# Performance work log

Measured on AMD Instinct MI355X. Metric: run time of the kernel, lower is better.

Reference implementation:

```python
import jax, jax.numpy as jnp
import numpy as np

EMB = 64
HID = 128
N_NODES = 50000
N_EDGES = 800000
N_Q = 64

def setup_inputs() -> dict:
    key = jax.random.key(0)
    ks = jax.random.split(key, 20)
    d = {}
    d['question_emb'] = jax.random.normal(ks[0], (N_Q, EMB), dtype=jnp.float32)
    d['node_embeddings'] = jax.random.normal(ks[1], (N_NODES, EMB), dtype=jnp.float32)
    d['edge_embeddings'] = jax.random.normal(ks[2], (N_EDGES, EMB), dtype=jnp.float32)
    d['edge_index'] = jax.random.randint(ks[3], (2, N_EDGES), 0, N_NODES, dtype=jnp.int32)
    d['node_batch'] = jnp.sort(jax.random.randint(ks[4], (N_NODES,), 0, N_Q, dtype=jnp.int32))
    s = 1.0 / np.sqrt(EMB)
    # projector weights (Linear emb->emb), stored as (in, out)
    d['Wq'] = jax.random.normal(ks[5], (EMB, EMB), dtype=jnp.float32) * s
    d['bq'] = jnp.zeros((EMB,), dtype=jnp.float32)
    d['We'] = jax.random.normal(ks[6], (EMB, EMB), dtype=jnp.float32) * s
    d['be'] = jnp.zeros((EMB,), dtype=jnp.float32)
    d['Wr'] = jax.random.normal(ks[7], (EMB, EMB), dtype=jnp.float32) * s
    d['br'] = jnp.zeros((EMB,), dtype=jnp.float32)
    # DenseFeatureExtractor: concat(4*EMB) -> EMB -> HID, ReLU after each
    d['W1'] = jax.random.normal(ks[8], (4 * EMB, EMB), dtype=jnp.float32) / np.sqrt(4 * EMB)
    d['b1'] = jnp.zeros((EMB,), dtype=jnp.float32)
    d['W2'] = jax.random.normal(ks[9], (EMB, HID), dtype=jnp.float32) * s
    d['b2'] = jnp.zeros((HID,), dtype=jnp.float32)
    # DeterministicHead: HID -> 1
    d['Wh'] = jax.random.normal(ks[10], (HID, 1), dtype=jnp.float32) / np.sqrt(HID)
    d['bh'] = jnp.zeros((1,), dtype=jnp.float32)
    return d


def reference(question_emb, node_embeddings, edge_embeddings, edge_index, node_batch,
              Wq, bq, We, be, Wr, br, W1, b1, W2, b2, Wh, bh):
    head_idx, tail_idx = edge_index[0], edge_index[1]
    query_ids = node_batch[head_idx]                       # [E]
    # projections (applied to the small tables, then gathered per edge)
    q_repr = question_emb @ Wq + bq                        # [Q, D]
    node_repr = node_embeddings @ We + be                  # [N, D]
    rel_repr = edge_embeddings @ Wr + br                   # [E, D]
    semantic = jnp.concatenate([
        q_repr[query_ids], node_repr[head_idx], rel_repr, node_repr[tail_idx]
    ], axis=-1)                                            # [E, 4D]
    h = jax.nn.relu(semantic @ W1 + b1)                    # [E, D]
    h = jax.nn.relu(h @ W2 + b2)                           # [E, H]
    logits = (h @ Wh + bh)[:, 0]                           # [E]
    scores = jax.nn.sigmoid(logits)
    return scores
```

## Files before the change

### kernel.cpp

```cpp
#include <hip/hip_runtime.h>

#define NNODE 50000
#define NEDGE 800000

typedef __attribute__((ext_vector_type(8))) short bf16x8;
typedef __attribute__((ext_vector_type(4))) float f32x4;

#define WB_QCB   0
#define WB_WRTB  8192
#define WB_W2TB  16384
#define WB_WEH   33024
#define WB_WET   49408
#define WB_NHB   65792
#define WB_NTB   6465792

__device__ inline ushort f2b(float x) {
    uint u = __float_as_uint(x);
    return (ushort)((u + 0x7fffu + ((u >> 16) & 1u)) >> 16);
}
__device__ inline uint cvtpk(float lo, float hi) {
    uint r;
    asm("v_cvt_pk_bf16_f32 %0, %1, %2" : "=v"(r) : "v"(lo), "v"(hi));
    return r;
}
__device__ inline float bLo(uint u) { return __uint_as_float(u << 16); }
__device__ inline float bHi(uint u) { return __uint_as_float(u & 0xffff0000u); }

__device__ inline void stage64(float* dst, const float* __restrict__ src, int t) {
    #pragma unroll
    for (int i = 0; i < 4; ++i) {
        int f = t + i * 256;
        *(float4*)&dst[f * 4] = *(const float4*)&src[f * 4];
    }
}

__device__ inline void gemm64(const float* sA, const float* sB, int t, float acc[4][4]) {
    const int r0 = (t >> 4) * 4, c0 = (t & 15) * 4;
    #pragma unroll
    for (int j = 0; j < 4; ++j)
        #pragma unroll
        for (int i = 0; i < 4; ++i) acc[j][i] = 0.f;
    #pragma unroll 4
    for (int k = 0; k < 64; ++k) {
        float4 b = *(const float4*)&sB[k * 64 + c0];
        float bv[4] = {b.x, b.y, b.z, b.w};
        #pragma unroll
        for (int j = 0; j < 4; ++j) {
            float a = sA[(r0 + j) * 64 + k];
            #pragma unroll
            for (int i = 0; i < 4; ++i) acc[j][i] = fmaf(a, bv[i], acc[j][i]);
        }
    }
}

__global__ __launch_bounds__(256)
void prep_small(const float* __restrict__ Q,
                const float* __restrict__ Wq, const float* __restrict__ bq,
                const float* __restrict__ We, const float* __restrict__ be,
                const float* __restrict__ Wr, const float* __restrict__ br,
                const float* __restrict__ W1, const float* __restrict__ b1,
                const float* __restrict__ W2, char* __restrict__ wsb)
{
    __shared__ float sA[4096], sB[4096], sC[4096], sBias[64];
    const int t = threadIdx.x;
    const int bid = blockIdx.x;
    const int r0 = (t >> 4) * 4, c0 = (t & 15) * 4;

    if (bid == 0) {
        stage64(sA, Wq, t); stage64(sB, W1, t);
        __syncthreads();
        float acc[4][4];
        gemm64(sA, sB, t, acc);
        #pragma unroll
        for (int j = 0; j < 4; ++j)
            *(float4*)&sC[(r0 + j) * 64 + c0] = make_float4(acc[j][0], acc[j][1], acc[j][2], acc[j][3]);
        if (t < 64) {
            float s = b1[t];
            for (int k = 0; k < 64; ++k) {
                s = fmaf(bq[k], W1[k * 64 + t], s);
                s = fmaf(be[k], W1[(64 + k) * 64 + t] + W1[(192 + k) * 64 + t], s);
                s = fmaf(br[k], W1[(128 + k) * 64 + t], s);
            }
            sBias[t] = s;
        }
        __syncthreads();
        stage64(sA, Q, t);
        __syncthreads();
        gemm64(sA, sC, t, acc);
        ushort* qcb = (ushort*)(wsb + WB_QCB);
        #pragma unroll
        for (int j = 0; j < 4; ++j) {
            ushort4 p;
            p.x = f2b(acc[j][0] + sBias[c0 + 0]);
            p.y = f2b(acc[j][1] + sBias[c0 + 1]);
            p.z = f2b(acc[j][2] + sBias[c0 + 2]);
            p.w = f2b(acc[j][3] + sBias[c0 + 3]);
            *(ushort4*)&qcb[(r0 + j) * 64 + c0] = p;
        }
    } else if (bid == 1 || bid == 2) {
        const float* w1seg = W1 + (bid == 1 ? 64 * 64 : 192 * 64);
        float* dst = (float*)(wsb + (bid == 1 ? WB_WEH : WB_WET));
        stage64(sA, We, t); stage64(sB, w1seg, t);
        __syncthreads();
        float acc[4][4];
        gemm64(sA, sB, t, acc);
        #pragma unroll
        for (int j = 0; j < 4; ++j)
            *(float4*)&dst[(r0 + j) * 64 + c0] = make_float4(acc[j][0], acc[j][1], acc[j][2], acc[j][3]);
    } else if (bid == 3) {
        stage64(sA, Wr, t); stage64(sB, W1 + 128 * 64, t);
        __syncthreads();
        float acc[4][4];
        gemm64(sA, sB, t, acc);
        ushort* wrtb = (ushort*)(wsb + WB_WRTB);
        #pragma unroll
        for (int j = 0; j < 4; ++j)
            #pragma unroll
            for (int i = 0; i < 4; ++i)
                wrtb[(c0 + i) * 64 + (r0 + j)] = f2b(acc[j][i]);
    } else {
        ushort* w2tb = (ushort*)(wsb + WB_W2TB);
        #pragma unroll
        for (int i = 0; i < 32; ++i) {
            int f = t + i * 256;
            int k = f >> 7, n = f & 127;
            w2tb[n * 64 + k] = f2b(W2[f]);
        }
    }
}

__global__ __launch_bounds__(256)
void prep_nodes(const float* __restrict__ Xn, const char* __restrict__ wsb_c,
                char* __restrict__ wsb)
{
    __shared__ float sXT[64 * 68];
    __shared__ float sWeh[4096], sWet[4096];
    const int t = threadIdx.x;
    const int nbase = blockIdx.x * 64;
    const float* Weh = (const float*)(wsb_c + WB_WEH);
    const float* Wet = (const float*)(wsb_c + WB_WET);
    ushort* nhb = (ushort*)(wsb + WB_NHB);
    ushort* ntb = (ushort*)(wsb + WB_NTB);

    #pragma unroll
    for (int i = 0; i < 4; ++i) {
        int f = t + i * 256;
        int n = f >> 4, s4 = (f & 15) * 4;
        int gn = nbase + n;
        float4 v = make_float4(0.f, 0.f, 0.f, 0.f);
        if (gn < NNODE) v = *(const float4*)&Xn[gn * 64 + s4];
        sXT[(s4 + 0) * 68 + n] = v.x;
        sXT[(s4 + 1) * 68 + n] = v.y;
        sXT[(s4 + 2) * 68 + n] = v.z;
        sXT[(s4 + 3) * 68 + n] = v.w;
    }
    #pragma unroll
    for (int i = 0; i < 4; ++i) {
        int f = t + i * 256;
        *(float4*)&sWeh[f * 4] = *(const float4*)&Weh[f * 4];
        *(float4*)&sWet[f * 4] = *(const float4*)&Wet[f * 4];
    }
    __syncthreads();

    const int er = (t >> 4) * 4, cc = (t & 15) * 4;
    float ah[4][4], at[4][4];
    #pragma unroll
    for (int j = 0; j < 4; ++j)
        #pragma unroll
        for (int i = 0; i < 4; ++i) { ah[j][i] = 0.f; at[j][i] = 0.f; }
    #pragma unroll 4
    for (int k = 0; k < 64; ++k) {
        float4 a  = *(const float4*)&sXT[k * 68 + er];
        float4 bh = *(const float4*)&sWeh[k * 64 + cc];
        float4 bt = *(const float4*)&sWet[k * 64 + cc];
        float av[4] = {a.x, a.y, a.z, a.w};
        #pragma unroll
        for (int j = 0; j < 4; ++j) {
            ah[j][0] = fmaf(av[j], bh.x, ah[j][0]); ah[j][1] = fmaf(av[j], bh.y, ah[j][1]);
            ah[j][2] = fmaf(av[j], bh.z, ah[j][2]); ah[j][3] = fmaf(av[j], bh.w, ah[j][3]);
            at[j][0] = fmaf(av[j], bt.x, at[j][0]); at[j][1] = fmaf(av[j], bt.y, at[j][1]);
            at[j][2] = fmaf(av[j], bt.z, at[j][2]); at[j][3] = fmaf(av[j], bt.w, at[j][3]);
        }
    }
    #pragma unroll
    for (int j = 0; j < 4; ++j) {
        int n = nbase + er + j;
        if (n < NNODE) {
            uint2 ph, pt;
            ph.x = cvtpk(ah[j][0], ah[j][1]); ph.y = cvtpk(ah[j][2], ah[j][3]);
            pt.x = cvtpk(at[j][0], at[j][1]); pt.y = cvtpk(at[j][2], at[j][3]);
            *(uint2*)&nhb[n * 64 + cc] = ph;
            *(uint2*)&ntb[n * 64 + cc] = pt;
        }
    }
}

#define TILES_PER_BLK 4

__global__ __launch_bounds__(256, 2)
void edge_kernel(const float* __restrict__ Xe,
                 const int* __restrict__ EI,
                 const int* __restrict__ NB,
                 const float* __restrict__ b2,
                 const float* __restrict__ Wh,
                 const float* __restrict__ bh,
                 const char* __restrict__ wsb,
                 float* __restrict__ out)
{
    __shared__ ushort sX[64 * 72];
    __shared__ ushort sG[64 * 72];

    const int t = threadIdx.x;
    const ushort* qcb  = (const ushort*)(wsb + WB_QCB);
    const ushort* wrtb = (const ushort*)(wsb + WB_WRTB);
    const ushort* w2tb = (const ushort*)(wsb + WB_W2TB);
    const ushort* nhb  = (const ushort*)(wsb + WB_NHB);
    const ushort* ntb  = (const ushort*)(wsb + WB_NTB);

    const int lane = t & 63;
    const int w    = t >> 6;
    const int m    = lane & 15;
    const int qq   = lane >> 4;
    const int q8   = qq * 8;

    const int eg  = t >> 2;
    const int c0g = (t & 3) * 16;
    const int xrow = 16 * w + (lane >> 2);
    const int xsl  = lane & 3;

    bf16x8 wrF[4][2], w2F[8][2];
    #pragma unroll
    for (int nt = 0; nt < 4; ++nt) {
        wrF[nt][0] = *(const bf16x8*)&wrtb[(nt * 16 + m) * 64 + q8];
        wrF[nt][1] = *(const bf16x8*)&wrtb[(nt * 16 + m) * 64 + 32 + q8];
    }
    #pragma unroll
    for (int nt = 0; nt < 8; ++nt) {
        w2F[nt][0] = *(const bf16x8*)&w2tb[(nt * 16 + m) * 64 + q8];
        w2F[nt][1] = *(const bf16x8*)&w2tb[(nt * 16 + m) * 64 + 32 + q8];
    }
    float b2v[8], whv[8];
    #pragma unroll
    for (int nt = 0; nt < 8; ++nt) {
        b2v[nt] = b2[nt * 16 + m];
        whv[nt] = Wh[nt * 16 + m];
    }
    const float bh0 = bh[0];

    auto load_tile = [&](int eb, uint4* g, float4* x) {
        int hd = EI[eb + eg];
        int tl = EI[NEDGE + eb + eg];
        int qi = NB[hd];
        g[0] = *(const uint4*)&qcb[qi * 64 + c0g];
        g[1] = *(const uint4*)&qcb[qi * 64 + c0g + 8];
        g[2] = *(const uint4*)&nhb[hd * 64 + c0g];
        g[3] = *(const uint4*)&nhb[hd * 64 + c0g + 8];
        g[4] = *(const uint4*)&ntb[tl * 64 + c0g];
        g[5] = *(const uint4*)&ntb[tl * 64 + c0g + 8];
        #pragma unroll
        for (int i = 0; i < 4; ++i)
            x[i] = *(const float4*)&Xe[(eb + xrow) * 64 + (xsl + 4 * i) * 4];
    };

    int ebase = blockIdx.x * (64 * TILES_PER_BLK);
    uint4  g[6];  float4 x[4];
    uint4  ng[6]; float4 nx[4];
    load_tile(ebase, g, x);

    #pragma unroll
    for (int tile = 0; tile < TILES_PER_BLK; ++tile) {
        {
            uint pk[8];
            const uint* ua = (const uint*)&g[0];
            const uint* ub = (const uint*)&g[2];
            const uint* uc = (const uint*)&g[4];
            #pragma unroll
            for (int j = 0; j < 4; ++j) {
                float lo = bLo(ua[j]) + bLo(ub[j]) + bLo(uc[j]);
                float hi = bHi(ua[j]) + bHi(ub[j]) + bHi(uc[j]);
                pk[j] = cvtpk(lo, hi);
            }
            ua = (const uint*)&g[1]; ub = (const uint*)&g[3]; uc = (const uint*)&g[5];
            #pragma unroll
            for (int j = 0; j < 4; ++j) {
                float lo = bLo(ua[j]) + bLo(ub[j]) + bLo(uc[j]);
                float hi = bHi(ua[j]) + bHi(ub[j]) + bHi(uc[j]);
                pk[4 + j] = cvtpk(lo, hi);
            }
            *(uint4*)&sG[eg * 72 + c0g]     = make_uint4(pk[0], pk[1], pk[2], pk[3]);
            *(uint4*)&sG[eg * 72 + c0g + 8] = make_uint4(pk[4], pk[5], pk[6], pk[7]);
        }
        #pragma unroll
        for (int i = 0; i < 4; ++i) {
            uint lo = cvtpk(x[i].x, x[i].y);
            uint hi = cvtpk(x[i].z, x[i].w);
            *(uint2*)&sX[xrow * 72 + (xsl + 4 * i) * 4] = make_uint2(lo, hi);
        }
        if (tile < TILES_PER_BLK - 1) load_tile(ebase + 64, ng, nx);

        bf16x8 a0 = *(const bf16x8*)&sX[(w * 16 + m) * 72 + q8];
        bf16x8 a1 = *(const bf16x8*)&sX[(w * 16 + m) * 72 + 32 + q8];
        f32x4 acc1[4];
        #pragma unroll
        for (int nt = 0; nt < 4; ++nt) {
            f32x4 c = {0.f, 0.f, 0.f, 0.f};
            c = __builtin_amdgcn_mfma_f32_16x16x32_bf16(a0, wrF[nt][0], c, 0, 0, 0);
            c = __builtin_amdgcn_mfma_f32_16x16x32_bf16(a1, wrF[nt][1], c, 0, 0, 0);
            acc1[nt] = c;
        }
        #pragma unroll
        for (int nt = 0; nt < 4; ++nt) {
            int c = nt * 16 + m;
            const int e0 = w * 16 + qq * 4;
            float v0 = fmaxf(acc1[nt][0] + __uint_as_float(((uint)sG[(e0 + 0) * 72 + c]) << 16), 0.f);
            float v1 = fmaxf(acc1[nt][1] + __uint_as_float(((uint)sG[(e0 + 1) * 72 + c]) << 16), 0.f);
            float v2 = fmaxf(acc1[nt][2] + __uint_as_float(((uint)sG[(e0 + 2) * 72 + c]) << 16), 0.f);
            float v3 = fmaxf(acc1[nt][3] + __uint_as_float(((uint)sG[(e0 + 3) * 72 + c]) << 16), 0.f);
            uint p01 = cvtpk(v0, v1);
            uint p23 = cvtpk(v2, v3);
            sX[(e0 + 0) * 72 + c] = (ushort)p01;
            sX[(e0 + 1) * 72 + c] = (ushort)(p01 >> 16);
            sX[(e0 + 2) * 72 + c] = (ushort)p23;
            sX[(e0 + 3) * 72 + c] = (ushort)(p23 >> 16);
        }

        bf16x8 A0 = *(const bf16x8*)&sX[(w * 16 + m) * 72 + q8];
        bf16x8 A1 = *(const bf16x8*)&sX[(w * 16 + m) * 72 + 32 + q8];
        float part[4] = {0.f, 0.f, 0.f, 0.f};
        #pragma unroll
        for (int nt = 0; nt < 8; ++nt) {
            f32x4 c = {0.f, 0.f, 0.f, 0.f};
            c = __builtin_amdgcn_mfma_f32_16x16x32_bf16(A0, w2F[nt][0], c, 0, 0, 0);
            c = __builtin_amdgcn_mfma_f32_16x16x32_bf16(A1, w2F[nt][1], c, 0, 0, 0);
            #pragma unroll
            for (int r = 0; r < 4; ++r)
                part[r] = fmaf(fmaxf(c[r] + b2v[nt], 0.f), whv[nt], part[r]);
        }
        #pragma unroll
        for (int md = 1; md < 16; md <<= 1) {
            part[0] += __shfl_xor(part[0], md, 64);
            part[1] += __shfl_xor(part[1], md, 64);
            part[2] += __shfl_xor(part[2], md, 64);
            part[3] += __shfl_xor(part[3], md, 64);
        }
        if (m == 0) {
            float4 o;
            o.x = 1.f / (1.f + __expf(-(part[0] + bh0)));
            o.y = 1.f / (1.f + __expf(-(part[1] + bh0)));
            o.z = 1.f / (1.f + __expf(-(part[2] + bh0)));
            o.w = 1.f / (1.f + __expf(-(part[3] + bh0)));
            *(float4*)&out[ebase + w * 16 + qq * 4] = o;
        }

        if (tile < TILES_PER_BLK - 1) {
            ebase += 64;
            #pragma unroll
            for (int i = 0; i < 6; ++i) g[i] = ng[i];
            #pragma unroll
            for (int i = 0; i < 4; ++i) x[i] = nx[i];
        }
    }
}

extern "C" void kernel_launch(void* const* d_in, const int* in_sizes, int n_in,
                              void* d_out, int out_size, void* d_ws, size_t ws_size,
                              hipStream_t stream)
{
    const float* Q   = (const float*)d_in[0];
    const float* Xn  = (const float*)d_in[1];
    const float* Xe  = (const float*)d_in[2];
    const int*   EI  = (const int*)d_in[3];
    const int*   NB  = (const int*)d_in[4];
    const float* Wq  = (const float*)d_in[5];
    const float* bq  = (const float*)d_in[6];
    const float* We  = (const float*)d_in[7];
    const float* be  = (const float*)d_in[8];
    const float* Wr  = (const float*)d_in[9];
    const float* br  = (const float*)d_in[10];
    const float* W1  = (const float*)d_in[11];
    const float* b1  = (const float*)d_in[12];
    const float* W2  = (const float*)d_in[13];
    const float* b2  = (const float*)d_in[14];
    const float* Wh  = (const float*)d_in[15];
    const float* bh  = (const float*)d_in[16];
    float* out = (float*)d_out;
    char*  wsb = (char*)d_ws;

    prep_small<<<5, 256, 0, stream>>>(Q, Wq, bq, We, be, Wr, br, W1, b1, W2, wsb);
    prep_nodes<<<(NNODE + 63) / 64, 256, 0, stream>>>(Xn, wsb, wsb);
    edge_kernel<<<NEDGE / (64 * TILES_PER_BLK), 256, 0, stream>>>(Xe, EI, NB, b2, Wh, bh, wsb, out);
}
```

Baseline: 376.2 us.

## Move W2 weights to LDS, drop register double-buffer, raise occupancy

The second-layer weight fragments, b2 and Wh move out of per-thread registers into shared memory, loaded cooperatively once per block before a barrier. The separate next-tile register buffers are removed, and the next tile's loads go straight into the current buffers after those are consumed. Launch bounds rise from 2 to 4 blocks per CU, aiming for more resident waves to hide gather latency. In exchange, each tile adds LDS reads for the W2 fragments and per-column bias/weight, and LDS use per block grows (sG padding also changes to a 68 stride).

```diff
diff --git a/kernel.cpp b/kernel.cpp
--- a/kernel.cpp
+++ b/kernel.cpp
@@ -197,7 +197,7 @@
 
 #define TILES_PER_BLK 4
 
-__global__ __launch_bounds__(256, 2)
+__global__ __launch_bounds__(256, 4)
 void edge_kernel(const float* __restrict__ Xe,
                  const int* __restrict__ EI,
                  const int* __restrict__ NB,
@@ -208,7 +208,9 @@
                  float* __restrict__ out)
 {
     __shared__ ushort sX[64 * 72];
-    __shared__ ushort sG[64 * 72];
+    __shared__ ushort sW2[128 * 72];
+    __shared__ ushort sG[64 * 68];
+    __shared__ float  sB2s[128], sWhs[128];
 
     const int t = threadIdx.x;
     const ushort* qcb  = (const ushort*)(wsb + WB_QCB);
@@ -228,24 +230,29 @@
     const int xrow = 16 * w + (lane >> 2);
     const int xsl  = lane & 3;
 
-    bf16x8 wrF[4][2], w2F[8][2];
+    bf16x8 wrF[4][2];
     #pragma unroll
     for (int nt = 0; nt < 4; ++nt) {
         wrF[nt][0] = *(const bf16x8*)&wrtb[(nt * 16 + m) * 64 + q8];
         wrF[nt][1] = *(const bf16x8*)&wrtb[(nt * 16 + m) * 64 + 32 + q8];
     }
-    #pragma unroll
-    for (int nt = 0; nt < 8; ++nt) {
-        w2F[nt][0] = *(const bf16x8*)&w2tb[(nt * 16 + m) * 64 + q8];
-        w2F[nt][1] = *(const bf16x8*)&w2tb[(nt * 16 + m) * 64 + 32 + q8];
-    }
-    float b2v[8], whv[8];
-    #pragma unroll
-    for (int nt = 0; nt < 8; ++nt) {
-        b2v[nt] = b2[nt * 16 + m];
-        whv[nt] = Wh[nt * 16 + m];
-    }
+    {
+        uint4 w2l[4];
+        #pragma unroll
+        for (int i = 0; i < 4; ++i) {
+            int f = t + i * 256;
+            w2l[i] = *(const uint4*)&w2tb[(f >> 3) * 64 + (f & 7) * 8];
+        }
+        #pragma unroll
+        for (int i = 0; i < 4; ++i) {
+            int f = t + i * 256;
+            *(uint4*)&sW2[(f >> 3) * 72 + (f & 7) * 8] = w2l[i];
+        }
+    }
+    if (t < 128) { sB2s[t] = b2[t]; sWhs[t] = Wh[t]; }
     const float bh0 = bh[0];
+
+    __syncthreads();
 
     auto load_tile = [&](int eb, uint4* g, float4* x) {
         int hd = EI[eb + eg];
@@ -263,8 +270,7 @@
     };
 
     int ebase = blockIdx.x * (64 * TILES_PER_BLK);
-    uint4  g[6];  float4 x[4];
-    uint4  ng[6]; float4 nx[4];
+    uint4 g[6]; float4 x[4];
     load_tile(ebase, g, x);
 
     #pragma unroll
@@ -287,8 +293,10 @@
                 float hi = bHi(ua[j]) + bHi(ub[j]) + bHi(uc[j]);
                 pk[4 + j] = cvtpk(lo, hi);
             }
-            *(uint4*)&sG[eg * 72 + c0g]     = make_uint4(pk[0], pk[1], pk[2], pk[3]);
-            *(uint4*)&sG[eg * 72 + c0g + 8] = make_uint4(pk[4], pk[5], pk[6], pk[7]);
+            *(uint2*)&sG[eg * 68 + c0g + 0 ] = make_uint2(pk[0], pk[1]);
+            *(uint2*)&sG[eg * 68 + c0g + 4 ] = make_uint2(pk[2], pk[3]);
+            *(uint2*)&sG[eg * 68 + c0g + 8 ] = make_uint2(pk[4], pk[5]);
+            *(uint2*)&sG[eg * 68 + c0g + 12] = make_uint2(pk[6], pk[7]);
         }
         #pragma unroll
         for (int i = 0; i < 4; ++i) {
@@ -296,7 +304,7 @@
             uint hi = cvtpk(x[i].z, x[i].w);
             *(uint2*)&sX[xrow * 72 + (xsl + 4 * i) * 4] = make_uint2(lo, hi);
         }
-        if (tile < TILES_PER_BLK - 1) load_tile(ebase + 64, ng, nx);
+        if (tile < TILES_PER_BLK - 1) load_tile(ebase + 64, g, x);
 
         bf16x8 a0 = *(const bf16x8*)&sX[(w * 16 + m) * 72 + q8];
         bf16x8 a1 = *(const bf16x8*)&sX[(w * 16 + m) * 72 + 32 + q8];
@@ -312,10 +320,10 @@
         for (int nt = 0; nt < 4; ++nt) {
             int c = nt * 16 + m;
             const int e0 = w * 16 + qq * 4;
-            float v0 = fmaxf(acc1[nt][0] + __uint_as_float(((uint)sG[(e0 + 0) * 72 + c]) << 16), 0.f);
-            float v1 = fmaxf(acc1[nt][1] + __uint_as_float(((uint)sG[(e0 + 1) * 72 + c]) << 16), 0.f);
-            float v2 = fmaxf(acc1[nt][2] + __uint_as_float(((uint)sG[(e0 + 2) * 72 + c]) << 16), 0.f);
-            float v3 = fmaxf(acc1[nt][3] + __uint_as_float(((uint)sG[(e0 + 3) * 72 + c]) << 16), 0.f);
+            float v0 = fmaxf(acc1[nt][0] + __uint_as_float(((uint)sG[(e0 + 0) * 68 + c]) << 16), 0.f);
+            float v1 = fmaxf(acc1[nt][1] + __uint_as_float(((uint)sG[(e0 + 1) * 68 + c]) << 16), 0.f);
+            float v2 = fmaxf(acc1[nt][2] + __uint_as_float(((uint)sG[(e0 + 2) * 68 + c]) << 16), 0.f);
+            float v3 = fmaxf(acc1[nt][3] + __uint_as_float(((uint)sG[(e0 + 3) * 68 + c]) << 16), 0.f);
             uint p01 = cvtpk(v0, v1);
             uint p23 = cvtpk(v2, v3);
             sX[(e0 + 0) * 72 + c] = (ushort)p01;
@@ -329,12 +337,16 @@
         float part[4] = {0.f, 0.f, 0.f, 0.f};
         #pragma unroll
         for (int nt = 0; nt < 8; ++nt) {
+            bf16x8 B0 = *(const bf16x8*)&sW2[(nt * 16 + m) * 72 + q8];
+            bf16x8 B1 = *(const bf16x8*)&sW2[(nt * 16 + m) * 72 + 32 + q8];
             f32x4 c = {0.f, 0.f, 0.f, 0.f};
-            c = __builtin_amdgcn_mfma_f32_16x16x32_bf16(A0, w2F[nt][0], c, 0, 0, 0);
-            c = __builtin_amdgcn_mfma_f32_16x16x32_bf16(A1, w2F[nt][1], c, 0, 0, 0);
+            c = __builtin_amdgcn_mfma_f32_16x16x32_bf16(A0, B0, c, 0, 0, 0);
+            c = __builtin_amdgcn_mfma_f32_16x16x32_bf16(A1, B1, c, 0, 0, 0);
+            int col = nt * 16 + m;
+            float b2v = sB2s[col], whv = sWhs[col];
             #pragma unroll
             for (int r = 0; r < 4; ++r)
-                part[r] = fmaf(fmaxf(c[r] + b2v[nt], 0.f), whv[nt], part[r]);
+                part[r] = fmaf(fmaxf(c[r] + b2v, 0.f), whv, part[r]);
         }
         #pragma unroll
         for (int md = 1; md < 16; md <<= 1) {
@@ -352,13 +364,7 @@
             *(float4*)&out[ebase + w * 16 + qq * 4] = o;
         }
 
-        if (tile < TILES_PER_BLK - 1) {
-            ebase += 64;
-            #pragma unroll
-            for (int i = 0; i < 6; ++i) g[i] = ng[i];
-            #pragma unroll
-            for (int i = 0; i < 4; ++i) x[i] = nx[i];
-        }
+        if (tile < TILES_PER_BLK - 1) ebase += 64;
     }
 }
 
```

Result: no change. 378.8 us (+0.7%).
